# Kernel optimization log

Hardware: AMD Instinct MI355X
Metric: run time of the kernel (lower is better)

The kernel has to match this reference:

```python
import jax, jax.numpy as jnp
import numpy as np

EPS = 1e-5
C, FR, T = 256, 7, 251  # channel, frequency, time
B = 32


def _bn(x, p, axis):
    # p: stacked [gamma, beta, running_mean, running_var] (eval-mode BatchNorm)
    g, b, m, v = p
    scale = g * jax.lax.rsqrt(v + EPS)
    shape = [1] * x.ndim
    shape[axis] = -1
    return x * scale.reshape(shape) + (b - m * scale).reshape(shape)


def _branch(xr, qw, qbn, kw, kbn, lbn):
    # xr: [N, Cin, L]. conv1x1 (no bias) + BN1d over channel axis.
    q = _bn(jnp.einsum('oc,ncl->nol', qw, xr), qbn, 1)
    k = _bn(jnp.einsum('oc,ncl->nol', kw, xr), kbn, 1)
    # adaptive_avg_pool2d((1, L)) on [N,1,Cin,L]: mean over channel axis, identity on L
    qv = q.mean(axis=1)  # [N, L]
    kv = k.mean(axis=1)  # [N, L]
    logits = qv[:, :, None] * kv[:, None, :]  # outer product == matmul(q^T, k): [N, L, L]
    g, b, m, v = lbn[:, 0]  # BatchNorm2d(1), eval mode -> scalar affine
    scale = g * jax.lax.rsqrt(v + EPS)
    w = jax.nn.softmax(logits * scale + (b - m * scale), axis=-1)
    # einsum 'bhxy,ihh->bhxy' == v * sum_i diag(w_i); return the diagonal sum [L]
    return jnp.einsum('nii->i', w)


def setup_inputs() -> dict:
    key = jax.random.key(0)
    ks = jax.random.split(key, 20)

    def w(k, o, i):
        return jax.random.normal(k, (o, i), jnp.float32) * 0.05

    def bn(k, n):
        k1, k2, k3, k4 = jax.random.split(k, 4)
        gamma = 1.0 + 0.1 * jax.random.normal(k1, (n,), jnp.float32)
        beta = 0.1 * jax.random.normal(k2, (n,), jnp.float32)
        mean = 0.1 * jax.random.normal(k3, (n,), jnp.float32)
        var = jnp.abs(1.0 + 0.1 * jax.random.normal(k4, (n,), jnp.float32))
        return jnp.stack([gamma, beta, mean, var])

    return {
        'x': jax.random.normal(ks[0], (B, C, FR, T), jnp.float32),
        'qc_w': w(ks[1], T, T), 'qc_bn': bn(ks[2], T),
        'kc_w': w(ks[3], T, T), 'kc_bn': bn(ks[4], T),
        'lc_bn': bn(ks[5], 1),
        'qf_w': w(ks[6], C, C), 'qf_bn': bn(ks[7], C),
        'kf_w': w(ks[8], C, C), 'kf_bn': bn(ks[9], C),
        'lf_bn': bn(ks[10], 1),
        'qt_w': w(ks[11], C, C), 'qt_bn': bn(ks[12], C),
        'kt_w': w(ks[13], C, C), 'kt_bn': bn(ks[14], C),
        'lt_bn': bn(ks[15], 1),
        'v_w': w(ks[16], C, C),
        'v_b': 0.05 * jax.random.normal(ks[17], (C,), jnp.float32),
        'v_bn': bn(ks[18], C),
    }


def reference(x, qc_w, qc_bn, kc_w, kc_bn, lc_bn,
              qf_w, qf_bn, kf_w, kf_bn, lf_bn,
              qt_w, qt_bn, kt_w, kt_bn, lt_bn,
              v_w, v_b, v_bn):
    b = x.shape[0]
    # x: [B, C, FR, T]
    x_c = x.transpose(0, 2, 3, 1).reshape(b * FR, T, C)   # conv over T channels
    x_f = x.transpose(0, 2, 1, 3).reshape(b * FR, C, T)   # conv over C channels
    x_t = x.transpose(0, 3, 1, 2).reshape(b * T, C, FR)   # conv over C channels
    dc = _branch(x_c, qc_w, qc_bn, kc_w, kc_bn, lc_bn)    # [C] (attention over channel axis of v)
    df = _branch(x_f, qf_w, qf_bn, kf_w, kf_bn, lf_bn)    # [T]
    dt = _branch(x_t, qt_w, qt_bn, kt_w, kt_bn, lt_bn)    # [FR]
    v = _bn(jnp.einsum('oc,bcxy->boxy', v_w, x) + v_b[None, :, None, None], v_bn, 1)
    # v_c + v_f + v_t + x, where each v_* = v scaled by summed attention diagonal
    return v * (dc[None, :, None, None] + dt[None, None, :, None] + df[None, None, None, :]) + x
```

## Files before the change

### kernel.cpp

```cpp
#include <hip/hip_runtime.h>

typedef unsigned short u16;
typedef __attribute__((ext_vector_type(8))) short short8;
typedef __attribute__((ext_vector_type(4))) float float4v;
typedef __attribute__((ext_vector_type(4))) int int4v;
typedef __attribute__((ext_vector_type(2))) int int2v;

#define EPS 1e-5f
#define NC 256
#define NT 251
#define NF 7
#define NSP 1757
#define NB 32

#define OFF_QEC 0
#define OFF_KEC 256
#define OFF_QEF 512
#define OFF_KEF 768
#define OFF_QET 1024
#define OFF_KET 1280
#define OFF_VSC 1536
#define OFF_VOF 1792
#define OFF_CONST 2048
#define OFF_DC 2064
#define OFF_DF 2320
#define OFF_DT 2576
#define WS_END 2592
#define OFF_QT 2592
#define OFF_KT (OFF_QT+56320)
#define WS2_END (OFF_KT+56320)
#define OFF_WB16 WS2_END
#define WS3_END (WS2_END+32768)
#define OFF_QF2 WS3_END
#define OFF_KF2 (OFF_QF2+56320)
#define OFF_QCS (OFF_KF2+56320)
#define OFF_KCS (OFF_QCS+57344)
#define WS4_END (OFF_KCS+57344)
#define OFF_XB16 WS4_END
#define XB16_U32 (448*16384)
#define WS5_END (OFF_XB16 + XB16_U32)

#define XSW(kg, w) ((kg)*256 + ((w) ^ ((((kg)>>1)&3)<<3)))

__device__ __forceinline__ u16 f2b(float f) {
    unsigned int u = __float_as_uint(f);
    return (u16)((u + 0x7FFFu + ((u >> 16) & 1u)) >> 16);
}
__device__ __forceinline__ unsigned int pk2(float a, float b) {
    return (unsigned int)f2b(a) | ((unsigned int)f2b(b) << 16);
}

__global__ __launch_bounds__(256) void prep_kernel(
    const float* qc_w, const float* qc_bn, const float* kc_w, const float* kc_bn, const float* lc_bn,
    const float* qf_w, const float* qf_bn, const float* kf_w, const float* kf_bn, const float* lf_bn,
    const float* qt_w, const float* qt_bn, const float* kt_w, const float* kt_bn, const float* lt_bn,
    const float* v_b, const float* v_bn, const float* v_w, float* ws)
{
    int tid = threadIdx.x;
    int blk = blockIdx.x;
    __shared__ float sc[256];
    __shared__ float red[256];
    if (blk < 24) {
        int m = blk >> 2, j = blk & 3;
        const float* w; const float* bn; float* out; int O;
        switch (m) {
            case 0: w=qc_w; bn=qc_bn; out=ws+OFF_QEC; O=NT; break;
            case 1: w=kc_w; bn=kc_bn; out=ws+OFF_KEC; O=NT; break;
            case 2: w=qf_w; bn=qf_bn; out=ws+OFF_QEF; O=NC; break;
            case 3: w=kf_w; bn=kf_bn; out=ws+OFF_KEF; O=NC; break;
            case 4: w=qt_w; bn=qt_bn; out=ws+OFF_QET; O=NC; break;
            default: w=kt_w; bn=kt_bn; out=ws+OFF_KET; O=NC; break;
        }
        if (tid < O) sc[tid] = bn[tid] * rsqrtf(bn[3*O+tid] + EPS);
        __syncthreads();
        int tl = tid & 63, kc4 = tid >> 6;
        int t = j*64 + tl;
        float acc = 0.f;
        if (t < O) {
            #pragma unroll 8
            for (int o = kc4; o < O; o += 4)
                acc = fmaf(sc[o], w[(size_t)o*O + t], acc);
        }
        red[tid] = acc;
        __syncthreads();
        if (tid < 64) {
            int tt = j*64 + tid;
            if (tt < O)
                out[tt] = (red[tid] + red[tid+64] + red[tid+128] + red[tid+192]) / (float)O;
        }
        if (j == 0) {
            float bs = 0.f;
            if (tid < O) bs = bn[O+tid] - bn[2*O+tid]*sc[tid];
            __syncthreads();
            red[tid] = bs; __syncthreads();
            for (int s2 = 128; s2 > 0; s2 >>= 1) { if (tid < s2) red[tid] += red[tid+s2]; __syncthreads(); }
            if (tid == 0) ws[OFF_CONST+m] = red[0] / (float)O;
        }
    } else if (blk == 24) {
        if (tid < NC) {
            float s = v_bn[tid] * rsqrtf(v_bn[3*NC+tid] + EPS);
            ws[OFF_VSC+tid] = s;
            ws[OFF_VOF+tid] = v_bn[NC+tid] - v_bn[2*NC+tid]*s + v_b[tid]*s;
        }
        if (tid == 0) {
            ws[OFF_CONST+6] = lc_bn[0] * rsqrtf(lc_bn[3] + EPS);
            ws[OFF_CONST+7] = lf_bn[0] * rsqrtf(lf_bn[3] + EPS);
            ws[OFF_CONST+8] = lt_bn[0] * rsqrtf(lt_bn[3] + EPS);
        }
        for (int i = tid; i < WS_END - OFF_DC; i += 256) ws[OFF_DC + i] = 0.f;
    } else {
        u16* wb = (u16*)(ws + OFF_WB16);
        int base = (blk - 25) * 8192;
        for (int i4 = tid; i4 < 2048; i4 += 256) {
            int e = base + i4*4;
            int o = e >> 8, k = e & 255;
            float4v v = *(const float4v*)(v_w + e);
            u16 h0 = f2b(v.x), h1 = f2b(v.y), h2 = f2b(v.z), h3 = f2b(v.w);
            int r = ((o>>7)<<3) | (k>>5);
            int q = (((o>>4)&7)<<9) | (((k>>3)&3)<<7) | ((o&15)<<3) | (k&7);
            unsigned long long pk = (unsigned long long)h0 | ((unsigned long long)h1<<16)
                                  | ((unsigned long long)h2<<32) | ((unsigned long long)h3<<48);
            *(unsigned long long*)&wb[(r<<12) | q] = pk;
        }
    }
}

__global__ __launch_bounds__(512) void qv_kernel(const float* __restrict__ x,
                                                 float* __restrict__ ws, int pack)
{
    __shared__ float lds[9760];
    int tid = threadIdx.x;
    int blk = blockIdx.x;
    const float* cst = ws + OFF_CONST;

    if (blk < 1792) {
        int n = blk >> 3, cb = blk & 7;
        int b = n / NF, f = n % NF;
        const float* xb = x + (size_t)b*NC*NSP + (size_t)f*NT + (size_t)(cb*32)*NSP;
        if (tid < NT) lds[8224+tid] = ws[OFF_QEC+tid];
        else if (tid >= 256 && tid < 256+NT) lds[8480+tid-256] = ws[OFF_KEC+tid-256];
        int lr = tid >> 8, lane = tid & 255;
        #pragma unroll 4
        for (int i = 0; i < 16; ++i) {
            int r = 2*i + lr;
            if (lane < NT) lds[r*257 + lane] = xb[(size_t)r*NSP + lane];
        }
        __syncthreads();
        int r = tid & 31, seg = tid >> 5;
        int t0 = seg*16, t1 = (seg == 15) ? NT : t0+16;
        float qa = 0.f, ka = 0.f;
        #pragma unroll 4
        for (int t = t0; t < t1; ++t) {
            float xv = lds[r*257 + t];
            qa = fmaf(lds[8224+t], xv, qa);
            ka = fmaf(lds[8480+t], xv, ka);
        }
        lds[8736 + seg*32 + r] = qa;
        lds[9248 + seg*32 + r] = ka;
        __syncthreads();
        if (tid < 64) {
            int rr = tid & 31, which = tid >> 5;
            int base = 8736 + which*512 + rr;
            float s = 0.f;
            #pragma unroll
            for (int sg = 0; sg < 16; ++sg) s += lds[base + sg*32];
            int ch = cb*32 + rr;
            if (which == 0) ws[OFF_QCS + n*256 + ch] = s;
            else            ws[OFF_KCS + n*256 + ch] = s;
        }
    } else {
        int fb = blk - 1792;
        int b = fb / 14, nchunk = fb % 14;
        int n0 = nchunk * 128;
        int spg = tid & 31, chg = tid >> 5;
        if (tid < 256) { lds[5120+tid] = ws[OFF_QEF+tid]; lds[5632+tid] = ws[OFF_QET+tid]; }
        else { int u = tid-256; lds[5376+u] = ws[OFF_KEF+u]; lds[5888+u] = ws[OFF_KET+u]; }
        __syncthreads();
        const size_t xbase = (size_t)b*NC*NSP;
        int sp0 = n0 + spg*4;
        bool full = (sp0 + 3 < NSP);
        unsigned int* ximg = nullptr;
        if (pack) ximg = (unsigned int*)(ws + OFF_XB16) + (size_t)(b*14 + nchunk)*16384;

        float qf[4]={0,0,0,0}, kf[4]={0,0,0,0}, qt[4]={0,0,0,0}, kt[4]={0,0,0,0};
        #pragma unroll
        for (int ii = 0; ii < 4; ++ii) {
            int ch0 = chg*16 + ii*4;
            float xv4[4][4];
            #pragma unroll
            for (int cc = 0; cc < 4; ++cc) {
                int ch = ch0 + cc;
                const float* xr = x + xbase + (size_t)ch*NSP + sp0;
                if (full) {
                    xv4[cc][0]=xr[0]; xv4[cc][1]=xr[1]; xv4[cc][2]=xr[2]; xv4[cc][3]=xr[3];
                } else {
                    #pragma unroll
                    for (int j = 0; j < 4; ++j) xv4[cc][j] = (sp0+j < NSP) ? xr[j] : 0.f;
                }
                float eqf = lds[5120+ch], ekf = lds[5376+ch];
                float eqt = lds[5632+ch], ekt = lds[5888+ch];
                #pragma unroll
                for (int j = 0; j < 4; ++j) {
                    qf[j] = fmaf(eqf, xv4[cc][j], qf[j]);
                    kf[j] = fmaf(ekf, xv4[cc][j], kf[j]);
                    qt[j] = fmaf(eqt, xv4[cc][j], qt[j]);
                    kt[j] = fmaf(ekt, xv4[cc][j], kt[j]);
                }
            }
            if (pack) {
                int kgsg = ch0 >> 2;
                int ks = kgsg >> 3, kgl = kgsg & 7;
                unsigned int* dst = ximg + ks*2048 + kgl*256 + spg*8;
                unsigned int pk[8];
                #pragma unroll
                for (int i = 0; i < 4; ++i) {
                    pk[i*2+0] = pk2(xv4[0][i], xv4[1][i]);
                    pk[i*2+1] = pk2(xv4[2][i], xv4[3][i]);
                }
                *(int4v*)&dst[0] = *(int4v*)&pk[0];
                *(int4v*)&dst[4] = *(int4v*)&pk[4];
            }
        }
        #pragma unroll
        for (int j = 0; j < 4; ++j) {
            qf[j] += __shfl_xor(qf[j], 32);
            kf[j] += __shfl_xor(kf[j], 32);
            qt[j] += __shfl_xor(qt[j], 32);
            kt[j] += __shfl_xor(kt[j], 32);
        }
        int wv = tid >> 6, ln = tid & 63;
        if (ln < 32) {
            #pragma unroll
            for (int j = 0; j < 4; ++j) {
                lds[(j)*256     + wv*32 + ln] = qf[j];
                lds[(4+j)*256   + wv*32 + ln] = kf[j];
                lds[(8+j)*256   + wv*32 + ln] = qt[j];
                lds[(12+j)*256  + wv*32 + ln] = kt[j];
            }
        }
        __syncthreads();
        if (tid < 32) {
            float acc[16];
            #pragma unroll
            for (int v = 0; v < 16; ++v) {
                float s = 0.f;
                #pragma unroll
                for (int w = 0; w < 8; ++w) s += lds[v*256 + w*32 + tid];
                acc[v] = s;
            }
            int sp0w = n0 + tid*4;
            #pragma unroll
            for (int j = 0; j < 4; ++j) {
                if (sp0w + j < NSP) {
                    size_t o = (size_t)b*1760 + sp0w + j;
                    ws[OFF_QF2 + o] = acc[j]    + cst[2];
                    ws[OFF_KF2 + o] = acc[4+j]  + cst[3];
                    ws[OFF_QT  + o] = acc[8+j]  + cst[4];
                    ws[OFF_KT  + o] = acc[12+j] + cst[5];
                }
            }
        }
    }
}

__global__ __launch_bounds__(256) void sm_kernel(float* __restrict__ ws)
{
    __shared__ float kv[NC];
    __shared__ float kv2[NT];
    __shared__ float dt_acc[NF];
    int tid = threadIdx.x, blk = blockIdx.x;
    const float* cst = ws + OFF_CONST;

    if (blk < 224) {
        int b = blk / NF, f = blk % NF;
        float qcv = ws[OFF_QCS + blk*256 + tid] + cst[0];
        float kcv = ws[OFF_KCS + blk*256 + tid] + cst[1];
        kv[tid] = kcv;
        float qfv = 0.f, kfv = 0.f;
        if (tid < NT) {
            size_t o = (size_t)b*1760 + f*NT + tid;
            qfv = ws[OFF_QF2 + o];
            kfv = ws[OFF_KF2 + o];
            kv2[tid] = kfv;
        }
        __syncthreads();
        {
            float s = cst[6];
            float qi = s * qcv;
            float m0=-1e30f, m1=-1e30f, m2=-1e30f, m3=-1e30f;
            #pragma unroll 2
            for (int jj = 0; jj < NC; jj += 4) {
                m0 = fmaxf(m0, qi*kv[jj]);
                m1 = fmaxf(m1, qi*kv[jj+1]);
                m2 = fmaxf(m2, qi*kv[jj+2]);
                m3 = fmaxf(m3, qi*kv[jj+3]);
            }
            float m = fmaxf(fmaxf(m0,m1), fmaxf(m2,m3));
            float d0=0.f, d1=0.f, d2=0.f, d3=0.f;
            #pragma unroll 2
            for (int jj = 0; jj < NC; jj += 4) {
                d0 += __expf(qi*kv[jj]   - m);
                d1 += __expf(qi*kv[jj+1] - m);
                d2 += __expf(qi*kv[jj+2] - m);
                d3 += __expf(qi*kv[jj+3] - m);
            }
            float den = (d0+d1)+(d2+d3);
            atomicAdd(&ws[OFF_DC + tid], __expf(qi*kcv - m)/den);
        }
        if (tid < NT) {
            float s = cst[7];
            float qi = s * qfv;
            float m0=-1e30f, m1=-1e30f, m2=-1e30f, m3=-1e30f;
            int jj = 0;
            #pragma unroll 2
            for (; jj + 3 < NT; jj += 4) {
                m0 = fmaxf(m0, qi*kv2[jj]);
                m1 = fmaxf(m1, qi*kv2[jj+1]);
                m2 = fmaxf(m2, qi*kv2[jj+2]);
                m3 = fmaxf(m3, qi*kv2[jj+3]);
            }
            for (; jj < NT; ++jj) m0 = fmaxf(m0, qi*kv2[jj]);
            float m = fmaxf(fmaxf(m0,m1), fmaxf(m2,m3));
            float d0=0.f, d1=0.f, d2=0.f, d3=0.f;
            jj = 0;
            #pragma unroll 2
            for (; jj + 3 < NT; jj += 4) {
                d0 += __expf(qi*kv2[jj]   - m);
                d1 += __expf(qi*kv2[jj+1] - m);
                d2 += __expf(qi*kv2[jj+2] - m);
                d3 += __expf(qi*kv2[jj+3] - m);
            }
            for (; jj < NT; ++jj) d0 += __expf(qi*kv2[jj] - m);
            float den = (d0+d1)+(d2+d3);
            atomicAdd(&ws[OFF_DF + tid], __expf(qi*kfv - m)/den);
        }
    } else {
        int b = blk - 224;
        if (tid < NF) dt_acc[tid] = 0.f;
        __syncthreads();
        if (tid < NT) {
            float s = cst[8];
            float q[NF], k[NF];
            #pragma unroll
            for (int i = 0; i < NF; ++i) {
                size_t o = (size_t)b*1760 + i*NT + tid;
                q[i] = ws[OFF_QT + o];
                k[i] = ws[OFF_KT + o];
            }
            #pragma unroll
            for (int i = 0; i < NF; ++i) {
                float qi = s * q[i];
                float m = -1e30f;
                #pragma unroll
                for (int j = 0; j < NF; ++j) m = fmaxf(m, qi*k[j]);
                float den = 0.f;
                #pragma unroll
                for (int j = 0; j < NF; ++j) den += __expf(qi*k[j] - m);
                atomicAdd(&dt_acc[i], __expf(qi*k[i] - m)/den);
            }
        }
        __syncthreads();
        if (tid < NF) atomicAdd(&ws[OFF_DT + tid], dt_acc[tid]);
    }
}

__global__ __launch_bounds__(512) void qkt_kernel(const float* __restrict__ x,
                                                  float* __restrict__ ws, int fuse_t)
{
    __shared__ float kv[NC];
    __shared__ float p0[512], p1[512], p2[512], p3[512];
    int tid = threadIdx.x;
    int bid = blockIdx.x;
    int n = bid >> 1, role = bid & 1;
    int b = n / NF, f = n % NF;
    const float* xb = x + (size_t)b*NC*NSP + (size_t)f*NT;
    const float* cst = ws + OFF_CONST;
    int half = tid >> 8, lid = tid & 255;

    if (role == 0) {
        const float* xrow = xb + (size_t)lid*NSP;
        const float* qeC = ws + OFF_QEC;  const float* keC = ws + OFF_KEC;
        float qc = 0.f, kc = 0.f;
        int t0 = half ? 126 : 0, t1 = half ? NT : 126;
        #pragma unroll 16
        for (int t = t0; t < t1; ++t) {
            float xv = xrow[t];
            qc = fmaf(qeC[t], xv, qc);
            kc = fmaf(keC[t], xv, kc);
        }
        p0[tid] = qc; p1[tid] = kc;
        __syncthreads();
        if (tid < 256) {
            qc = p0[tid] + p0[tid+256] + cst[0];
            kc = p1[tid] + p1[tid+256] + cst[1];
            kv[tid] = kc;
        }
        __syncthreads();
        if (tid < 256) {
            float s = cst[6];
            float qi = s * qc;
            float m0=-1e30f, m1=-1e30f, m2=-1e30f, m3=-1e30f;
            #pragma unroll 2
            for (int jj = 0; jj < NC; jj += 4) {
                m0 = fmaxf(m0, qi*kv[jj]);
                m1 = fmaxf(m1, qi*kv[jj+1]);
                m2 = fmaxf(m2, qi*kv[jj+2]);
                m3 = fmaxf(m3, qi*kv[jj+3]);
            }
            float m = fmaxf(fmaxf(m0,m1), fmaxf(m2,m3));
            float d0=0.f, d1=0.f, d2=0.f, d3=0.f;
            #pragma unroll 2
            for (int jj = 0; jj < NC; jj += 4) {
                d0 += __expf(qi*kv[jj]   - m);
                d1 += __expf(qi*kv[jj+1] - m);
                d2 += __expf(qi*kv[jj+2] - m);
                d3 += __expf(qi*kv[jj+3] - m);
            }
            float den = (d0+d1)+(d2+d3);
            atomicAdd(&ws[OFF_DC + tid], __expf(qi*kv[tid] - m)/den);
        }
    } else {
        float qf=0.f, kf=0.f, qt=0.f, kt=0.f;
        if (lid < NT) {
            const float* xc = xb + lid + (size_t)(half*128)*NSP;
            const float* qeF = ws + OFF_QEF + half*128;  const float* keF = ws + OFF_KEF + half*128;
            const float* qeT = ws + OFF_QET + half*128;  const float* keT = ws + OFF_KET + half*128;
            #pragma unroll 8
            for (int ch = 0; ch < 128; ++ch) {
                float xv = xc[(size_t)ch*NSP];
                qf = fmaf(qeF[ch], xv, qf);
                kf = fmaf(keF[ch], xv, kf);
                qt = fmaf(qeT[ch], xv, qt);
                kt = fmaf(keT[ch], xv, kt);
            }
        }
        p0[tid]=qf; p1[tid]=kf; p2[tid]=qt; p3[tid]=kt;
        __syncthreads();
        float qfv=0.f, kfv=0.f;
        if (tid < NT) {
            qfv = p0[tid] + p0[tid+256] + cst[2];
            kfv = p1[tid] + p1[tid+256] + cst[3];
            float qtv = p2[tid] + p2[tid+256] + cst[4];
            float ktv = p3[tid] + p3[tid+256] + cst[5];
            kv[tid] = kfv;
            if (fuse_t) {
                ws[OFF_QT + ((size_t)b*NT + tid)*NF + f] = qtv;
                ws[OFF_KT + ((size_t)b*NT + tid)*NF + f] = ktv;
            }
        }
        __syncthreads();
        if (tid < NT) {
            float s = cst[7];
            float qi = s * qfv;
            float m0=-1e30f, m1=-1e30f, m2=-1e30f, m3=-1e30f;
            int jj = 0;
            #pragma unroll 2
            for (; jj + 3 < NT; jj += 4) {
                m0 = fmaxf(m0, qi*kv[jj]);
                m1 = fmaxf(m1, qi*kv[jj+1]);
                m2 = fmaxf(m2, qi*kv[jj+2]);
                m3 = fmaxf(m3, qi*kv[jj+3]);
            }
            for (; jj < NT; ++jj) m0 = fmaxf(m0, qi*kv[jj]);
            float m = fmaxf(fmaxf(m0,m1), fmaxf(m2,m3));
            float d0=0.f, d1=0.f, d2=0.f, d3=0.f;
            jj = 0;
            #pragma unroll 2
            for (; jj + 3 < NT; jj += 4) {
                d0 += __expf(qi*kv[jj]   - m);
                d1 += __expf(qi*kv[jj+1] - m);
                d2 += __expf(qi*kv[jj+2] - m);
                d3 += __expf(qi*kv[jj+3] - m);
            }
            for (; jj < NT; ++jj) d0 += __expf(qi*kv[jj] - m);
            float den = (d0+d1)+(d2+d3);
            atomicAdd(&ws[OFF_DF + tid], __expf(qi*kfv - m)/den);
        }
    }
}

__global__ __launch_bounds__(256) void tsm_kernel(float* __restrict__ ws)
{
    __shared__ float dt_acc[NF];
    int tid = threadIdx.x, b = blockIdx.x;
    if (tid < NF) dt_acc[tid] = 0.f;
    __syncthreads();
    if (tid < NT) {
        float s = ws[OFF_CONST+8];
        const float* qp = ws + OFF_QT + ((size_t)b*NT + tid)*NF;
        const float* kp = ws + OFF_KT + ((size_t)b*NT + tid)*NF;
        float q[NF], k[NF];
        #pragma unroll
        for (int i = 0; i < NF; ++i) { q[i] = qp[i]; k[i] = kp[i]; }
        #pragma unroll
        for (int i = 0; i < NF; ++i) {
            float qi = s * q[i];
            float m = -1e30f;
            #pragma unroll
            for (int j = 0; j < NF; ++j) m = fmaxf(m, qi*k[j]);
            float den = 0.f;
            #pragma unroll
            for (int j = 0; j < NF; ++j) den += __expf(qi*k[j] - m);
            atomicAdd(&dt_acc[i], __expf(qi*k[i] - m)/den);
        }
    }
    __syncthreads();
    if (tid < NF) atomicAdd(&ws[OFF_DT + tid], dt_acc[tid]);
}

__global__ __launch_bounds__(256) void t_kernel(const float* __restrict__ x, float* __restrict__ ws)
{
    __shared__ float qs[32*NF], ks[32*NF], dt_acc[NF];
    int tid = threadIdx.x;
    int b  = blockIdx.x >> 3;
    int t0 = (blockIdx.x & 7) * 32;
    int tl = tid & 31, fr = tid >> 5;
    int t = t0 + tl;
    bool act = (fr < NF) && (t < NT);
    if (tid < NF) dt_acc[tid] = 0.f;

    float aq = 0.f, ak = 0.f;
    const float* qeT = ws + OFF_QET;
    const float* keT = ws + OFF_KET;
    if (act) {
        const float* xr = x + (size_t)b*NC*NSP + fr*NT + t;
        #pragma unroll 8
        for (int ch = 0; ch < NC; ++ch) {
            float xv = xr[(size_t)ch*NSP];
            aq = fmaf(qeT[ch], xv, aq);
            ak = fmaf(keT[ch], xv, ak);
        }
    }
    __syncthreads();
    if (act) {
        qs[tl*NF + fr] = aq + ws[OFF_CONST+4];
        ks[tl*NF + fr] = ak + ws[OFF_CONST+5];
    }
    __syncthreads();
    if (act) {
        float s = ws[OFF_CONST+8];
        float qi = s * qs[tl*NF + fr];
        float m = -1e30f;
        #pragma unroll
        for (int j = 0; j < NF; ++j) m = fmaxf(m, qi*ks[tl*NF + j]);
        float den = 0.f;
        #pragma unroll
        for (int j = 0; j < NF; ++j) den += __expf(qi*ks[tl*NF + j] - m);
        atomicAdd(&dt_acc[fr], __expf(qi*ks[tl*NF + fr] - m)/den);
    }
    __syncthreads();
    if (tid < NF) atomicAdd(&ws[OFF_DT + tid], dt_acc[tid]);
}

__global__ __launch_bounds__(256, 3) void main2_kernel(
    const float* __restrict__ x, const float* __restrict__ ws, float* __restrict__ out)
{
    __shared__ float vsL[128], voL[128], dcL[128], dtfL[128];
    int tid = threadIdx.x;
    int flat = blockIdx.x;
    int xcd = flat & 7, idx = flat >> 3;
    int pair = xcd*56 + (idx >> 1);
    int o0 = (idx & 1) * 128;
    int n0 = (pair % 14) * 128;
    int b  = pair / 14;
    const size_t xbase = (size_t)b * NC * NSP;

    float evs=0.f, evo=0.f, edc=0.f, edtf=0.f;
    if (tid < 128) {
        int o = o0 + tid;
        evs = ws[OFF_VSC+o];
        evo = ws[OFF_VOF+o];
        edc = ws[OFF_DC+o];
        int nn = n0 + tid; if (nn > NSP-1) nn = NSP-1;
        int ff = nn / NT, tt = nn - ff*NT;
        edtf = ws[OFF_DT+ff] + ws[OFF_DF+tt];
    }

    int wv = tid >> 6, ln = tid & 63;
    int quad = ln >> 4, l16 = ln & 15;
    int wr = wv >> 1, wc = wv & 1;

    const u16* wimg = (const u16*)(ws + OFF_WB16) + (size_t)(o0 >> 7) * 32768;
    const unsigned int* ximg = (const unsigned int*)(ws + OFF_XB16)
                             + (size_t)(b*14 + (n0 >> 7)) * 16384;

    float4v acc[4][4] = {};
    short8 afr[2][4];
    int2v blo[2][4], bhi[2][4];

    auto LF = [&](int ks, int s) {
        #pragma unroll
        for (int fr = 0; fr < 4; ++fr)
            afr[s][fr] = *(const short8*)&wimg[ks*4096 + (wr*4+fr)*512 + ln*8];
        #pragma unroll
        for (int fc = 0; fc < 4; ++fc) {
            int nn = wc*64 + fc*16 + l16;
            blo[s][fc] = *(const int2v*)&ximg[ks*2048 + (2*quad)*256 + 2*nn];
            bhi[s][fc] = *(const int2v*)&ximg[ks*2048 + (2*quad+1)*256 + 2*nn];
        }
    };

    LF(0, 0);
    #pragma unroll
    for (int ks = 0; ks < 8; ++ks) {
        const int cur = ks & 1;
        if (ks < 7) LF(ks+1, cur ^ 1);
        #pragma unroll
        for (int fc = 0; fc < 4; ++fc) {
            union { int i4[4]; short8 v; } u;
            u.i4[0] = blo[cur][fc].x; u.i4[1] = blo[cur][fc].y;
            u.i4[2] = bhi[cur][fc].x; u.i4[3] = bhi[cur][fc].y;
            short8 bv = u.v;
            #pragma unroll
            for (int fr = 0; fr < 4; ++fr)
                acc[fr][fc] = __builtin_amdgcn_mfma_f32_16x16x32_bf16(
                    afr[cur][fr], bv, acc[fr][fc], 0, 0, 0);
        }
    }

    if (tid < 128) { vsL[tid]=evs; voL[tid]=evo; dcL[tid]=edc; dtfL[tid]=edtf; }
    __syncthreads();

    #pragma unroll
    for (int fr = 0; fr < 4; ++fr) {
        #pragma unroll
        for (int r = 0; r < 4; ++r) {
            int ol = wr*64 + fr*16 + quad*4 + r;
            int o = o0 + ol;
            float vs = vsL[ol], vo = voL[ol], dcv = dcL[ol];
            const size_t orow = xbase + (size_t)o*NSP;
            #pragma unroll
            for (int fc = 0; fc < 4; ++fc) {
                int nl = wc*64 + fc*16 + l16;
                int nn = n0 + nl;
                if (nn < NSP) {
                    size_t gi = orow + nn;
                    out[gi] = (acc[fr][fc][r]*vs + vo)*(dcv + dtfL[nl]) + x[gi];
                }
            }
        }
    }
}

template<int WBF>
__global__ __launch_bounds__(256) void main_kernel(
    const float* __restrict__ x, const float* __restrict__ vw,
    const float* __restrict__ ws, float* __restrict__ out)
{
    __shared__ u16 Ws[2][4096];
    __shared__ unsigned int Xs[2][2048];
    __shared__ float vsL[128], voL[128], dcL[128], dtfL[128];

    int tid = threadIdx.x;
    int flat = blockIdx.x;
    int xcd = flat & 7, idx = flat >> 3;
    int pair = xcd*56 + (idx >> 1);
    int o0 = (idx & 1) * 128;
    int n0 = (pair % 14) * 128;
    int b  = pair / 14;
    const size_t xbase = (size_t)b * NC * NSP;

    if (tid < 128) {
        int o = o0 + tid;
        vsL[tid] = ws[OFF_VSC+o];
        voL[tid] = ws[OFF_VOF+o];
        dcL[tid] = ws[OFF_DC+o];
        int nn = n0 + tid; if (nn > NSP-1) nn = NSP-1;
        int ff = nn / NT, tt = nn - ff*NT;
        dtfL[tid] = ws[OFF_DT+ff] + ws[OFF_DF+tt];
    }

    int wv = tid >> 6, ln = tid & 63;
    int quad = ln >> 4, l16 = ln & 15;
    int wr = wv >> 1, wc = wv & 1;

    float4v acc[4][4] = {};

    int kgs = tid >> 5, nbs = tid & 31;
    int oo = tid >> 1, half = tid & 1;

    const u16* wbg = nullptr;
    if constexpr (WBF) wbg = (const u16*)(ws + OFF_WB16) + (size_t)(o0 >> 7) * 32768;

    int4v wA, wB;
    float wf[16];
    float xv[4][4];

    auto loadW = [&](int ks) {
        if constexpr (WBF) {
            const int4v* wsrc = (const int4v*)(wbg + (size_t)ks*4096);
            wA = wsrc[tid]; wB = wsrc[256 + tid];
        } else {
            const float* wr4 = vw + (size_t)(o0+oo)*NC + ks*32 + half*16;
            #pragma unroll
            for (int c = 0; c < 16; ++c) wf[c] = wr4[c];
        }
    };
    auto loadX = [&](int ks) {
        int nbase = n0 + nbs*4;
        const float* xr = x + xbase + (size_t)(ks*32 + kgs*4)*NSP + nbase;
        if (nbase + 3 < NSP) {
            #pragma unroll
            for (int rr = 0; rr < 4; ++rr)
                #pragma unroll
                for (int i = 0; i < 4; ++i)
                    xv[rr][i] = xr[(size_t)rr*NSP + i];
        } else {
            #pragma unroll
            for (int rr = 0; rr < 4; ++rr)
                #pragma unroll
                for (int i = 0; i < 4; ++i)
                    xv[rr][i] = (nbase + i < NSP) ? xr[(size_t)rr*NSP + i] : 0.f;
        }
    };
    auto storeWX = [&](int bufi) {
        if constexpr (WBF) {
            *(int4v*)&Ws[bufi][tid*8]        = wA;
            *(int4v*)&Ws[bufi][2048 + tid*8] = wB;
        } else {
            union { u16 us[16]; short8 v[2]; } wb;
            #pragma unroll
            for (int c = 0; c < 16; ++c) wb.us[c] = f2b(wf[c]);
            int frg = oo >> 4, o16 = oo & 15;
            #pragma unroll
            for (int qq = 0; qq < 2; ++qq) {
                int qd = 2*half + qq;
                *(short8*)&Ws[bufi][frg*512 + qd*128 + o16*8] = wb.v[qq];
            }
        }
        unsigned int pk[8];
        #pragma unroll
        for (int i = 0; i < 4; ++i)
            #pragma unroll
            for (int jp = 0; jp < 2; ++jp)
                pk[i*2+jp] = pk2(xv[2*jp][i], xv[2*jp+1][i]);
        *(int4v*)&Xs[bufi][XSW(kgs, nbs*8)]     = *(int4v*)&pk[0];
        *(int4v*)&Xs[bufi][XSW(kgs, nbs*8 + 4)] = *(int4v*)&pk[4];
    };

    loadW(0); loadX(0);
    storeWX(0);
    __syncthreads();

    for (int ks = 0; ks < 8; ++ks) {
        int cur = ks & 1;
        if (ks < 7) { loadW(ks+1); loadX(ks+1); }

        short8 afr[4], bfr[4];
        #pragma unroll
        for (int fr = 0; fr < 4; ++fr)
            afr[fr] = *(short8*)&Ws[cur][(wr*4+fr)*512 + ln*8];
        #pragma unroll
        for (int fc = 0; fc < 4; ++fc) {
            int nn = wc*64 + fc*16 + l16;
            int2v lo = *(int2v*)&Xs[cur][XSW(2*quad,   2*nn)];
            int2v hi = *(int2v*)&Xs[cur][XSW(2*quad+1, 2*nn)];
            union { int i4[4]; short8 v; } u;
            u.i4[0] = lo.x; u.i4[1] = lo.y; u.i4[2] = hi.x; u.i4[3] = hi.y;
            bfr[fc] = u.v;
        }
        #pragma unroll
        for (int fr = 0; fr < 4; ++fr)
            #pragma unroll
            for (int fc = 0; fc < 4; ++fc)
                acc[fr][fc] = __builtin_amdgcn_mfma_f32_16x16x32_bf16(
                    afr[fr], bfr[fc], acc[fr][fc], 0, 0, 0);

        if (ks < 7) storeWX(cur ^ 1);
        __syncthreads();
    }

    #pragma unroll
    for (int fr = 0; fr < 4; ++fr) {
        #pragma unroll
        for (int r = 0; r < 4; ++r) {
            int ol = wr*64 + fr*16 + quad*4 + r;
            int o = o0 + ol;
            float vs = vsL[ol], vo = voL[ol], dcv = dcL[ol];
            const size_t orow = xbase + (size_t)o*NSP;
            #pragma unroll
            for (int fc = 0; fc < 4; ++fc) {
                int nl = wc*64 + fc*16 + l16;
                int nn = n0 + nl;
                if (nn < NSP) {
                    size_t gi = orow + nn;
                    out[gi] = (acc[fr][fc][r]*vs + vo)*(dcv + dtfL[nl]) + x[gi];
                }
            }
        }
    }
}

extern "C" void kernel_launch(void* const* d_in, const int* in_sizes, int n_in,
                              void* d_out, int out_size, void* d_ws, size_t ws_size,
                              hipStream_t stream)
{
    const float* x    = (const float*)d_in[0];
    const float* qc_w = (const float*)d_in[1];  const float* qc_bn = (const float*)d_in[2];
    const float* kc_w = (const float*)d_in[3];  const float* kc_bn = (const float*)d_in[4];
    const float* lc_bn= (const float*)d_in[5];
    const float* qf_w = (const float*)d_in[6];  const float* qf_bn = (const float*)d_in[7];
    const float* kf_w = (const float*)d_in[8];  const float* kf_bn = (const float*)d_in[9];
    const float* lf_bn= (const float*)d_in[10];
    const float* qt_w = (const float*)d_in[11]; const float* qt_bn = (const float*)d_in[12];
    const float* kt_w = (const float*)d_in[13]; const float* kt_bn = (const float*)d_in[14];
    const float* lt_bn= (const float*)d_in[15];
    const float* v_w  = (const float*)d_in[16]; const float* v_b   = (const float*)d_in[17];
    const float* v_bn = (const float*)d_in[18];
    float* ws = (float*)d_ws;
    float* out = (float*)d_out;

    int fuse_t = (ws_size >= (size_t)WS2_END * sizeof(float)) ? 1 : 0;
    int wbf    = (ws_size >= (size_t)WS3_END * sizeof(float)) ? 1 : 0;
    int newq   = (ws_size >= (size_t)WS4_END * sizeof(float)) ? 1 : 0;
    int xb     = (ws_size >= (size_t)WS5_END * sizeof(float)) ? 1 : 0;

    prep_kernel<<<wbf ? 33 : 25, 256, 0, stream>>>(qc_w,qc_bn,kc_w,kc_bn,lc_bn,
                                                   qf_w,qf_bn,kf_w,kf_bn,lf_bn,
                                                   qt_w,qt_bn,kt_w,kt_bn,lt_bn,
                                                   v_b,v_bn,v_w,ws);
    if (newq) {
        qv_kernel<<<2240, 512, 0, stream>>>(x, ws, xb);
        sm_kernel<<<256, 256, 0, stream>>>(ws);
    } else {
        qkt_kernel<<<NB*NF*2, 512, 0, stream>>>(x, ws, fuse_t);
        if (fuse_t) tsm_kernel<<<NB, 256, 0, stream>>>(ws);
        else        t_kernel<<<NB*8, 256, 0, stream>>>(x, ws);
    }
    if (xb && wbf)
        main2_kernel<<<896, 256, 0, stream>>>(x, ws, out);
    else if (wbf)
        main_kernel<1><<<896, 256, 0, stream>>>(x, v_w, ws, out);
    else
        main_kernel<0><<<896, 256, 0, stream>>>(x, v_w, ws, out);
}
```

Before: 225.8 us.

## Split qv_kernel channel work across twice as many blocks with atomic accumulation

The frequency/time projection blocks now each handle half of the 256 channels. Partial sums are combined with atomicAdd into buffers that prep_kernel zeroes beforehand, and the BN constant offsets move into sm_kernel. The channel-branch blocks shrink from 32 to 16 channels, and shared memory per block drops, so more blocks can be resident at once. The aim is better occupancy and load balance for this bandwidth-bound pass, at the cost of extra atomic traffic, extra zeroing work and a second read of the shared weights.

```diff
diff --git a/kernel.cpp b/kernel.cpp
--- a/kernel.cpp
+++ b/kernel.cpp
@@ -54,7 +54,7 @@
     const float* qc_w, const float* qc_bn, const float* kc_w, const float* kc_bn, const float* lc_bn,
     const float* qf_w, const float* qf_bn, const float* kf_w, const float* kf_bn, const float* lf_bn,
     const float* qt_w, const float* qt_bn, const float* kt_w, const float* kt_bn, const float* lt_bn,
-    const float* v_b, const float* v_bn, const float* v_w, float* ws)
+    const float* v_b, const float* v_bn, const float* v_w, float* ws, int nz)
 {
     int tid = threadIdx.x;
     int blk = blockIdx.x;
@@ -108,7 +108,7 @@
             ws[OFF_CONST+8] = lt_bn[0] * rsqrtf(lt_bn[3] + EPS);
         }
         for (int i = tid; i < WS_END - OFF_DC; i += 256) ws[OFF_DC + i] = 0.f;
-    } else {
+    } else if (blk < 33) {
         u16* wb = (u16*)(ws + OFF_WB16);
         int base = (blk - 25) * 8192;
         for (int i4 = tid; i4 < 2048; i4 += 256) {
@@ -122,59 +122,42 @@
                                   | ((unsigned long long)h2<<32) | ((unsigned long long)h3<<48);
             *(unsigned long long*)&wb[(r<<12) | q] = pk;
         }
+    } else {
+        if (!nz) return;
+        int z = blk - 33;
+        float* p;
+        switch (z) {
+            case 0: p = ws + OFF_QF2; break;
+            case 1: p = ws + OFF_KF2; break;
+            case 2: p = ws + OFF_QT;  break;
+            default: p = ws + OFF_KT; break;
+        }
+        float4v zv = {0.f, 0.f, 0.f, 0.f};
+        for (int i = tid; i < 14080; i += 256) ((float4v*)p)[i] = zv;
     }
 }
 
 __global__ __launch_bounds__(512) void qv_kernel(const float* __restrict__ x,
                                                  float* __restrict__ ws, int pack)
 {
-    __shared__ float lds[9760];
+    __shared__ float lds[6144];
     int tid = threadIdx.x;
     int blk = blockIdx.x;
-    const float* cst = ws + OFF_CONST;
-
-    if (blk < 1792) {
-        int n = blk >> 3, cb = blk & 7;
-        int b = n / NF, f = n % NF;
-        const float* xb = x + (size_t)b*NC*NSP + (size_t)f*NT + (size_t)(cb*32)*NSP;
-        if (tid < NT) lds[8224+tid] = ws[OFF_QEC+tid];
-        else if (tid >= 256 && tid < 256+NT) lds[8480+tid-256] = ws[OFF_KEC+tid-256];
-        int lr = tid >> 8, lane = tid & 255;
-        #pragma unroll 4
-        for (int i = 0; i < 16; ++i) {
-            int r = 2*i + lr;
-            if (lane < NT) lds[r*257 + lane] = xb[(size_t)r*NSP + lane];
-        }
-        __syncthreads();
-        int r = tid & 31, seg = tid >> 5;
-        int t0 = seg*16, t1 = (seg == 15) ? NT : t0+16;
-        float qa = 0.f, ka = 0.f;
-        #pragma unroll 4
-        for (int t = t0; t < t1; ++t) {
-            float xv = lds[r*257 + t];
-            qa = fmaf(lds[8224+t], xv, qa);
-            ka = fmaf(lds[8480+t], xv, ka);
-        }
-        lds[8736 + seg*32 + r] = qa;
-        lds[9248 + seg*32 + r] = ka;
-        __syncthreads();
-        if (tid < 64) {
-            int rr = tid & 31, which = tid >> 5;
-            int base = 8736 + which*512 + rr;
-            float s = 0.f;
-            #pragma unroll
-            for (int sg = 0; sg < 16; ++sg) s += lds[base + sg*32];
-            int ch = cb*32 + rr;
-            if (which == 0) ws[OFF_QCS + n*256 + ch] = s;
-            else            ws[OFF_KCS + n*256 + ch] = s;
-        }
-    } else {
-        int fb = blk - 1792;
-        int b = fb / 14, nchunk = fb % 14;
+
+    if (blk < 896) {
+        int half = blk & 1;
+        int pairid = blk >> 1;
+        int b = pairid / 14, nchunk = pairid % 14;
         int n0 = nchunk * 128;
         int spg = tid & 31, chg = tid >> 5;
-        if (tid < 256) { lds[5120+tid] = ws[OFF_QEF+tid]; lds[5632+tid] = ws[OFF_QET+tid]; }
-        else { int u = tid-256; lds[5376+u] = ws[OFF_KEF+u]; lds[5888+u] = ws[OFF_KET+u]; }
+        if (tid < 128) {
+            lds[4096+tid] = ws[OFF_QEF + half*128 + tid];
+            lds[4352+tid] = ws[OFF_QET + half*128 + tid];
+        } else if (tid < 256) {
+            int u = tid - 128;
+            lds[4224+u] = ws[OFF_KEF + half*128 + u];
+            lds[4480+u] = ws[OFF_KET + half*128 + u];
+        }
         __syncthreads();
         const size_t xbase = (size_t)b*NC*NSP;
         int sp0 = n0 + spg*4;
@@ -184,8 +167,9 @@
 
         float qf[4]={0,0,0,0}, kf[4]={0,0,0,0}, qt[4]={0,0,0,0}, kt[4]={0,0,0,0};
         #pragma unroll
-        for (int ii = 0; ii < 4; ++ii) {
-            int ch0 = chg*16 + ii*4;
+        for (int ii = 0; ii < 2; ++ii) {
+            int chl0 = chg*8 + ii*4;
+            int ch0 = half*128 + chl0;
             float xv4[4][4];
             #pragma unroll
             for (int cc = 0; cc < 4; ++cc) {
@@ -197,8 +181,8 @@
                     #pragma unroll
                     for (int j = 0; j < 4; ++j) xv4[cc][j] = (sp0+j < NSP) ? xr[j] : 0.f;
                 }
-                float eqf = lds[5120+ch], ekf = lds[5376+ch];
-                float eqt = lds[5632+ch], ekt = lds[5888+ch];
+                float eqf = lds[4096+chl0+cc], ekf = lds[4224+chl0+cc];
+                float eqt = lds[4352+chl0+cc], ekt = lds[4480+chl0+cc];
                 #pragma unroll
                 for (int j = 0; j < 4; ++j) {
                     qf[j] = fmaf(eqf, xv4[cc][j], qf[j]);
@@ -253,12 +237,48 @@
             for (int j = 0; j < 4; ++j) {
                 if (sp0w + j < NSP) {
                     size_t o = (size_t)b*1760 + sp0w + j;
-                    ws[OFF_QF2 + o] = acc[j]    + cst[2];
-                    ws[OFF_KF2 + o] = acc[4+j]  + cst[3];
-                    ws[OFF_QT  + o] = acc[8+j]  + cst[4];
-                    ws[OFF_KT  + o] = acc[12+j] + cst[5];
+                    atomicAdd(&ws[OFF_QF2 + o], acc[j]);
+                    atomicAdd(&ws[OFF_KF2 + o], acc[4+j]);
+                    atomicAdd(&ws[OFF_QT  + o], acc[8+j]);
+                    atomicAdd(&ws[OFF_KT  + o], acc[12+j]);
                 }
             }
+        }
+    } else {
+        int blk2 = blk - 896;
+        int n = blk2 >> 4, cb = blk2 & 15;
+        int b = n / NF, f = n % NF;
+        const float* xb = x + (size_t)b*NC*NSP + (size_t)f*NT + (size_t)(cb*16)*NSP;
+        if (tid < NT) lds[4112+tid] = ws[OFF_QEC+tid];
+        else if (tid >= 256 && tid < 256+NT) lds[4368+tid-256] = ws[OFF_KEC+tid-256];
+        int lr = tid >> 8, lane = tid & 255;
+        #pragma unroll
+        for (int i = 0; i < 8; ++i) {
+            int r = 2*i + lr;
+            if (lane < NT) lds[r*257 + lane] = xb[(size_t)r*NSP + lane];
+        }
+        __syncthreads();
+        int r = tid & 15, seg = tid >> 4;
+        int t0 = seg*8, t1 = (seg == 31) ? NT : t0+8;
+        float qa = 0.f, ka = 0.f;
+        #pragma unroll 8
+        for (int t = t0; t < t1; ++t) {
+            float xv = lds[r*257 + t];
+            qa = fmaf(lds[4112+t], xv, qa);
+            ka = fmaf(lds[4368+t], xv, ka);
+        }
+        lds[4624 + seg*16 + r] = qa;
+        lds[5136 + seg*16 + r] = ka;
+        __syncthreads();
+        if (tid < 32) {
+            int rr = tid & 15, which = tid >> 4;
+            int base = (which ? 5136 : 4624) + rr;
+            float s = 0.f;
+            #pragma unroll
+            for (int sg = 0; sg < 32; ++sg) s += lds[base + sg*16];
+            int ch = cb*16 + rr;
+            if (which == 0) ws[OFF_QCS + n*256 + ch] = s;
+            else            ws[OFF_KCS + n*256 + ch] = s;
         }
     }
 }
@@ -279,8 +299,8 @@
         float qfv = 0.f, kfv = 0.f;
         if (tid < NT) {
             size_t o = (size_t)b*1760 + f*NT + tid;
-            qfv = ws[OFF_QF2 + o];
-            kfv = ws[OFF_KF2 + o];
+            qfv = ws[OFF_QF2 + o] + cst[2];
+            kfv = ws[OFF_KF2 + o] + cst[3];
             kv2[tid] = kfv;
         }
         __syncthreads();
@@ -344,8 +364,8 @@
             #pragma unroll
             for (int i = 0; i < NF; ++i) {
                 size_t o = (size_t)b*1760 + i*NT + tid;
-                q[i] = ws[OFF_QT + o];
-                k[i] = ws[OFF_KT + o];
+                q[i] = ws[OFF_QT + o] + cst[4];
+                k[i] = ws[OFF_KT + o] + cst[5];
             }
             #pragma unroll
             for (int i = 0; i < NF; ++i) {
@@ -815,12 +835,12 @@
     int newq   = (ws_size >= (size_t)WS4_END * sizeof(float)) ? 1 : 0;
     int xb     = (ws_size >= (size_t)WS5_END * sizeof(float)) ? 1 : 0;
 
-    prep_kernel<<<wbf ? 33 : 25, 256, 0, stream>>>(qc_w,qc_bn,kc_w,kc_bn,lc_bn,
+    prep_kernel<<<wbf ? 37 : 25, 256, 0, stream>>>(qc_w,qc_bn,kc_w,kc_bn,lc_bn,
                                                    qf_w,qf_bn,kf_w,kf_bn,lf_bn,
                                                    qt_w,qt_bn,kt_w,kt_bn,lt_bn,
-                                                   v_b,v_bn,v_w,ws);
+                                                   v_b,v_bn,v_w,ws,newq);
     if (newq) {
-        qv_kernel<<<2240, 512, 0, stream>>>(x, ws, xb);
+        qv_kernel<<<4480, 512, 0, stream>>>(x, ws, xb);
         sm_kernel<<<256, 256, 0, stream>>>(ws);
     } else {
         qkt_kernel<<<NB*NF*2, 512, 0, stream>>>(x, ws, fuse_t);
```

Result: faster. 215.2 us (-4.7%).
